# Optimization experiments

Hardware: AMD Instinct MI355X
Metric: run time of the kernel (lower is better)

## Reference

```python
import jax, jax.numpy as jnp
import numpy as np

N_NODES = 100000


def setup_inputs() -> dict:
    key = jax.random.key(0)
    k1, k2, k3, k4 = jax.random.split(key, 4)
    h = jax.random.normal(k1, (N_NODES, 128), dtype=jnp.float32)
    src = jax.random.randint(k2, (1600000,), 0, N_NODES, dtype=jnp.int32)
    dst = jax.random.randint(k3, (1600000,), 0, N_NODES, dtype=jnp.int32)
    # Linear params (PyTorch default init scale ~ 1/sqrt(in_feats))
    W = jax.random.normal(k4, (128, 128), dtype=jnp.float32) * (1.0 / np.sqrt(128.0))
    b = jnp.zeros((128,), dtype=jnp.float32)
    return {"h": h, "src": src, "dst": dst, "W": W, "b": b}


def reference(h, src, dst, W, b):
    # fn.copy_src: gather source-node features per edge  [E, F]
    msgs = h[src]
    # fn.sum: scatter-add messages into destination nodes  [N, F]
    agg = jax.ops.segment_sum(msgs, dst, num_segments=h.shape[0])
    # NodeUpdateModule: linear + relu
    out = agg @ W.T + b
    return jax.nn.relu(out)
```

## Files before the change

### kernel.cpp

```cpp
#include <hip/hip_runtime.h>

#define F      128
#define NPB    256
#define NPBS   8
#define NBMAX  512
#define ECAP   5120
#define CHMAX  4096
#define CH_PT  4
#define OVFCAP 32768
#define BR     64
#define KC     32

typedef short bf16x8 __attribute__((ext_vector_type(8)));
typedef float f32x4  __attribute__((ext_vector_type(4)));

__device__ __forceinline__ unsigned short f32_to_bf16_rne(float x) {
    unsigned u = __float_as_uint(x);
    u += 0x7fffu + ((u >> 16) & 1u);
    return (unsigned short)(u >> 16);
}
__device__ __forceinline__ float bf16_to_f32(unsigned short u) {
    return __uint_as_float((unsigned)u << 16);
}

__global__ __launch_bounds__(256) void conv_w_kernel(
        const float* __restrict__ Wf, unsigned short* __restrict__ Wb, int n4) {
    int i = blockIdx.x * blockDim.x + threadIdx.x;
    if (i < n4) {
        float4 v = *(const float4*)(Wf + 4 * (long)i);
        ushort4 o;
        o.x = f32_to_bf16_rne(v.x);
        o.y = f32_to_bf16_rne(v.y);
        o.z = f32_to_bf16_rne(v.z);
        o.w = f32_to_bf16_rne(v.w);
        *(ushort4*)(Wb + 4 * (long)i) = o;
    }
}

__global__ __launch_bounds__(256) void gemm_h_kernel(
        const float* __restrict__ h,
        const unsigned short* __restrict__ Wb,
        unsigned short* __restrict__ hp,
        int n_rows) {
    const int wave = (blockIdx.x * 256 + threadIdx.x) >> 6;
    const int lane = threadIdx.x & 63;
    const int m0 = wave * 16;
    if (m0 >= n_rows) return;
    const int mn   = lane & 15;
    const int quad = lane >> 4;

    const int rowc = min(m0 + mn, n_rows - 1);
    const float* arow = h + (long)rowc * F + quad * 8;

    bf16x8 afr[4];
    #pragma unroll
    for (int kk = 0; kk < 4; ++kk) {
        float4 p0 = *(const float4*)(arow + kk * 32);
        float4 p1 = *(const float4*)(arow + kk * 32 + 4);
        bf16x8 f;
        f[0] = (short)f32_to_bf16_rne(p0.x);
        f[1] = (short)f32_to_bf16_rne(p0.y);
        f[2] = (short)f32_to_bf16_rne(p0.z);
        f[3] = (short)f32_to_bf16_rne(p0.w);
        f[4] = (short)f32_to_bf16_rne(p1.x);
        f[5] = (short)f32_to_bf16_rne(p1.y);
        f[6] = (short)f32_to_bf16_rne(p1.z);
        f[7] = (short)f32_to_bf16_rne(p1.w);
        afr[kk] = f;
    }

    f32x4 acc[8];
    #pragma unroll
    for (int t = 0; t < 8; ++t) acc[t] = (f32x4){0.f, 0.f, 0.f, 0.f};

    #pragma unroll
    for (int kk = 0; kk < 4; ++kk) {
        #pragma unroll
        for (int t = 0; t < 8; ++t) {
            const unsigned short* wp = Wb + (long)(t * 16 + mn) * F + kk * 32 + quad * 8;
            bf16x8 bfr = *(const bf16x8*)wp;
            acc[t] = __builtin_amdgcn_mfma_f32_16x16x32_bf16(afr[kk], bfr, acc[t], 0, 0, 0);
        }
    }

    #pragma unroll
    for (int t = 0; t < 8; ++t) {
        const int col = t * 16 + mn;
        #pragma unroll
        for (int r = 0; r < 4; ++r) {
            const int orow = m0 + quad * 4 + r;
            if (orow < n_rows)
                hp[(long)orow * F + col] = f32_to_bf16_rne(acc[t][r]);
        }
    }
}

__global__ __launch_bounds__(1024) void count_kernel(
        const int* __restrict__ dst,
        int* __restrict__ cntmat,
        int n_edges, int NB) {
    __shared__ int hist[NBMAX];
    const int tid = threadIdx.x;
    const int lo = blockIdx.x * CHMAX;
    const int hi = min(n_edges, lo + CHMAX);
    for (int i = tid; i < NB; i += 1024) hist[i] = 0;
    __syncthreads();
    for (int i = lo + tid; i < hi; i += 1024)
        atomicAdd(&hist[((unsigned)dst[i]) >> NPBS], 1);
    __syncthreads();
    int* row = cntmat + (long)blockIdx.x * NB;
    for (int i = tid; i < NB; i += 1024) row[i] = hist[i];
}

__global__ __launch_bounds__(256) void scan_kernel(
        int* __restrict__ cntmat, int* __restrict__ gcnt, int NB, int NBLK) {
    __shared__ int wsum[4];
    const int b = blockIdx.x;
    const int tid = threadIdx.x;
    const int lane = tid & 63;
    const int w = tid >> 6;
    int carry = 0;
    for (int c0 = 0; c0 < NBLK; c0 += 256) {
        const int blk = c0 + tid;
        const int own = (blk < NBLK) ? cntmat[(long)blk * NB + b] : 0;
        int v = own;
        #pragma unroll
        for (int d = 1; d < 64; d <<= 1) { int u = __shfl_up(v, d); if (lane >= d) v += u; }
        if (lane == 63) wsum[w] = v;
        __syncthreads();
        if (w == 0) {
            int s = (lane < 4) ? wsum[lane] : 0;
            #pragma unroll
            for (int d = 1; d < 4; d <<= 1) { int u = __shfl_up(s, d); if (lane >= d) s += u; }
            if (lane < 4) wsum[lane] = s;
        }
        __syncthreads();
        const int excl = v - own + ((w > 0) ? wsum[w - 1] : 0) + carry;
        if (blk < NBLK) cntmat[(long)blk * NB + b] = excl;
        carry += wsum[3];
        __syncthreads();
    }
    if (tid == 0) gcnt[b] = carry;
}

__global__ __launch_bounds__(1024) void scatter_kernel(
        const int* __restrict__ src,
        const int* __restrict__ dst,
        const int* __restrict__ cntmat,
        int* __restrict__ ebuf,
        int* __restrict__ ovf,
        int n_edges, int NB) {
    __shared__ int hist[NBMAX];
    __shared__ int dlt[NBMAX];
    __shared__ int cursor[NBMAX];
    __shared__ int sval[CHMAX];
    __shared__ unsigned short sbkt[CHMAX];
    __shared__ int wsum[16];
    const int tid = threadIdx.x;
    const int lane = tid & 63;
    const int w = tid >> 6;
    const int lo = blockIdx.x * CHMAX;
    const int hi = min(n_edges, lo + CHMAX);
    const int len = hi - lo;

    int dd[CH_PT], ss[CH_PT];
    #pragma unroll
    for (int k = 0; k < CH_PT; ++k) {
        int i = lo + k * 1024 + tid;
        bool ok = i < hi;
        dd[k] = ok ? dst[i] : -1;
        ss[k] = ok ? src[i] : 0;
    }
    for (int i = tid; i < NB; i += 1024) hist[i] = 0;
    __syncthreads();

    #pragma unroll
    for (int k = 0; k < CH_PT; ++k)
        if (dd[k] >= 0) atomicAdd(&hist[((unsigned)dd[k]) >> NPBS], 1);
    __syncthreads();

    const int own = (tid < NB) ? hist[tid] : 0;
    int v = own;
    #pragma unroll
    for (int d = 1; d < 64; d <<= 1) { int u = __shfl_up(v, d); if (lane >= d) v += u; }
    if (lane == 63) wsum[w] = v;
    __syncthreads();
    if (w == 0) {
        int s = (lane < 16) ? wsum[lane] : 0;
        #pragma unroll
        for (int d = 1; d < 16; d <<= 1) { int u = __shfl_up(s, d); if (lane >= d) s += u; }
        if (lane < 16) wsum[lane] = s;
    }
    __syncthreads();
    if (tid < NB) {
        const int excl = v - own + ((w > 0) ? wsum[w - 1] : 0);
        dlt[tid] = cntmat[(long)blockIdx.x * NB + tid] - excl;
        cursor[tid] = excl;
    }
    __syncthreads();

    #pragma unroll
    for (int k = 0; k < CH_PT; ++k)
        if (dd[k] >= 0) {
            int b = ((unsigned)dd[k]) >> NPBS;
            int p = atomicAdd(&cursor[b], 1);
            sval[p] = ((dd[k] & (NPB - 1)) << 20) | ss[k];
            sbkt[p] = (unsigned short)b;
        }
    __syncthreads();

    for (int i = tid; i < len; i += 1024) {
        int vv = sval[i];
        int b = sbkt[i];
        int slot = i + dlt[b];
        if (slot < ECAP) {
            ebuf[(long)b * ECAP + slot] = vv;
        } else {
            int q = atomicAdd(&ovf[0], 1);
            if (q < OVFCAP) {
                ovf[1 + 2 * q] = (b << NPBS) | (vv >> 20);
                ovf[2 + 2 * q] = vv & 0xFFFFF;
            }
        }
    }
}

__global__ __launch_bounds__(1024) void bucket_gather_kernel(
        const unsigned short* __restrict__ hp,
        const int* __restrict__ gcnt,
        const int* __restrict__ ebuf,
        const int* __restrict__ ovf,
        const float* __restrict__ bias,
        float* __restrict__ out,
        int n_nodes) {
    __shared__ int hist[NPB];
    __shared__ int ofs[NPB];
    __shared__ int cur[NPB];
    __shared__ int srt[ECAP];
    __shared__ int wsum[16];
    const int bkt = blockIdx.x;
    const int tid = threadIdx.x;
    const int lane = tid & 63;
    const int w = tid >> 6;
    const int cnt = min(gcnt[bkt], ECAP);
    const int novf = ovf[0];
    const int* eb = ebuf + (long)bkt * ECAP;

    int ev[5];
    #pragma unroll
    for (int k = 0; k < 5; ++k) {
        int i = k * 1024 + tid;
        ev[k] = (i < cnt) ? eb[i] : -1;
    }
    if (tid < NPB) hist[tid] = 0;
    __syncthreads();

    #pragma unroll
    for (int k = 0; k < 5; ++k)
        if (ev[k] >= 0) atomicAdd(&hist[((unsigned)ev[k]) >> 20], 1);
    __syncthreads();

    const int own = (tid < NPB) ? hist[tid] : 0;
    int v = own;
    #pragma unroll
    for (int d = 1; d < 64; d <<= 1) { int u = __shfl_up(v, d); if (lane >= d) v += u; }
    if (lane == 63) wsum[w] = v;
    __syncthreads();
    if (w == 0) {
        int s = (lane < 16) ? wsum[lane] : 0;
        #pragma unroll
        for (int d = 1; d < 16; d <<= 1) { int u = __shfl_up(s, d); if (lane >= d) s += u; }
        if (lane < 16) wsum[lane] = s;
    }
    __syncthreads();
    if (tid < NPB) {
        const int e = v - own + ((w > 0) ? wsum[w - 1] : 0);
        ofs[tid] = e;
        cur[tid] = e;
    }
    __syncthreads();

    #pragma unroll
    for (int k = 0; k < 5; ++k)
        if (ev[k] >= 0) {
            int p = atomicAdd(&cur[((unsigned)ev[k]) >> 20], 1);
            srt[p] = ev[k] & 0xFFFFF;
        }
    __syncthreads();

    const unsigned lo4 = lane << 2;
    const float2 bv = *(const float2*)(bias + (lane << 1));
    for (int nl = w; nl < NPB; nl += 16) {
        const int n = (bkt << NPBS) + nl;
        if (n >= n_nodes) break;
        const int beg = ofs[nl];
        const int end = beg + hist[nl];

        float ax = 0.f, ay = 0.f;
        for (int i = beg; i < end; i += 8) {
            unsigned vv[8]; bool val[8];
            #pragma unroll
            for (int j = 0; j < 8; ++j) {
                val[j] = (i + j) < end;
                int sid = srt[val[j] ? i + j : beg];
                unsigned bo = ((unsigned)sid << 8) | lo4;
                vv[j] = *(const unsigned*)((const char*)hp + bo);
            }
            #pragma unroll
            for (int j = 0; j < 8; ++j) {
                if (val[j]) {
                    ax += __uint_as_float(vv[j] << 16);
                    ay += __uint_as_float(vv[j] & 0xffff0000u);
                }
            }
        }

        if (novf > 0) {
            int ne = min(novf, OVFCAP);
            for (int k = 0; k < ne; ++k) {
                if (ovf[1 + 2 * k] == n) {
                    int s = ovf[2 + 2 * k];
                    unsigned bo = ((unsigned)s << 8) | lo4;
                    unsigned u = *(const unsigned*)((const char*)hp + bo);
                    ax += __uint_as_float(u << 16);
                    ay += __uint_as_float(u & 0xffff0000u);
                }
            }
        }

        float rx = fmaxf(ax + bv.x, 0.f);
        float ry = fmaxf(ay + bv.y, 0.f);
        unsigned oo = ((unsigned)n << 9) | (lane << 3);
        *(float2*)((char*)out + oo) = make_float2(rx, ry);
    }
}

__global__ void scatter_add_kernel(const float* __restrict__ h,
                                   const int* __restrict__ src,
                                   const int* __restrict__ dst,
                                   float* __restrict__ agg,
                                   long total) {
    long stride = (long)gridDim.x * blockDim.x;
    for (long i = (long)blockIdx.x * blockDim.x + threadIdx.x; i < total; i += stride) {
        int e    = (int)(i >> 5);
        int lane = (int)(i & 31);
        int s = src[e];
        int d = dst[e];
        float4 v = *(const float4*)(h + (long)s * F + (lane << 2));
        float* o = agg + (long)d * F + (lane << 2);
        unsafeAtomicAdd(o + 0, v.x);
        unsafeAtomicAdd(o + 1, v.y);
        unsafeAtomicAdd(o + 2, v.z);
        unsafeAtomicAdd(o + 3, v.w);
    }
}

__global__ __launch_bounds__(256) void gemm_bias_relu_inplace(
        float* __restrict__ out,
        const float* __restrict__ W,
        const float* __restrict__ bias,
        int n_rows) {
    __shared__ __align__(16) float a_t[KC][BR + 4];
    __shared__ __align__(16) float w_t[KC][F + 4];
    const int tid = threadIdx.x;
    const int tx = tid & 15;
    const int ty = tid >> 4;
    const int row0 = blockIdx.x * BR;
    float acc[4][8];
    #pragma unroll
    for (int i = 0; i < 4; ++i)
        #pragma unroll
        for (int j = 0; j < 8; ++j) acc[i][j] = 0.f;
    for (int kc = 0; kc < F; kc += KC) {
        #pragma unroll
        for (int p = 0; p < 2; ++p) {
            int q = tid + p * 256, r = q >> 3, kq = q & 7;
            int row = row0 + r;
            float4 v = make_float4(0.f, 0.f, 0.f, 0.f);
            if (row < n_rows) v = *(const float4*)(out + (long)row * F + kc + (kq << 2));
            a_t[kq * 4 + 0][r] = v.x; a_t[kq * 4 + 1][r] = v.y;
            a_t[kq * 4 + 2][r] = v.z; a_t[kq * 4 + 3][r] = v.w;
        }
        #pragma unroll
        for (int p = 0; p < 4; ++p) {
            int q = tid + p * 256, j = q >> 3, kq = q & 7;
            float4 v = *(const float4*)(W + (long)j * F + kc + (kq << 2));
            w_t[kq * 4 + 0][j] = v.x; w_t[kq * 4 + 1][j] = v.y;
            w_t[kq * 4 + 2][j] = v.z; w_t[kq * 4 + 3][j] = v.w;
        }
        __syncthreads();
        #pragma unroll
        for (int k = 0; k < KC; ++k) {
            float4 av = *(const float4*)&a_t[k][ty << 2];
            float4 w0 = *(const float4*)&w_t[k][tx << 2];
            float4 w1 = *(const float4*)&w_t[k][64 + (tx << 2)];
            float a4[4] = {av.x, av.y, av.z, av.w};
            float wv[8] = {w0.x, w0.y, w0.z, w0.w, w1.x, w1.y, w1.z, w1.w};
            #pragma unroll
            for (int i = 0; i < 4; ++i)
                #pragma unroll
                for (int j = 0; j < 8; ++j) acc[i][j] += a4[i] * wv[j];
        }
        __syncthreads();
    }
    float4 b0 = *(const float4*)(bias + (tx << 2));
    float4 b1 = *(const float4*)(bias + 64 + (tx << 2));
    #pragma unroll
    for (int i = 0; i < 4; ++i) {
        int row = row0 + (ty << 2) + i;
        if (row < n_rows) {
            float4 r0, r1;
            r0.x = fmaxf(acc[i][0] + b0.x, 0.f); r0.y = fmaxf(acc[i][1] + b0.y, 0.f);
            r0.z = fmaxf(acc[i][2] + b0.z, 0.f); r0.w = fmaxf(acc[i][3] + b0.w, 0.f);
            r1.x = fmaxf(acc[i][4] + b1.x, 0.f); r1.y = fmaxf(acc[i][5] + b1.y, 0.f);
            r1.z = fmaxf(acc[i][6] + b1.z, 0.f); r1.w = fmaxf(acc[i][7] + b1.w, 0.f);
            *(float4*)(out + (long)row * F + (tx << 2)) = r0;
            *(float4*)(out + (long)row * F + 64 + (tx << 2)) = r1;
        }
    }
}

extern "C" void kernel_launch(void* const* d_in, const int* in_sizes, int n_in,
                              void* d_out, int out_size, void* d_ws, size_t ws_size,
                              hipStream_t stream) {
    const float* h   = (const float*)d_in[0];
    const int*   src = (const int*)d_in[1];
    const int*   dst = (const int*)d_in[2];
    const float* W   = (const float*)d_in[3];
    const float* b   = (const float*)d_in[4];
    float* out = (float*)d_out;

    const int n_nodes = in_sizes[0] / F;
    const int n_edges = in_sizes[1];
    const int NB   = (n_nodes + NPB - 1) >> NPBS;
    const int NBLK = (n_edges + CHMAX - 1) / CHMAX;

    auto al16 = [](size_t x) { return (x + 15) & ~(size_t)15; };
    const size_t off_gcnt = 0;
    const size_t off_ovf  = al16((size_t)NB * 4);
    const size_t off_cmat = al16(off_ovf + 4 + (size_t)OVFCAP * 8);
    const size_t off_ebuf = al16(off_cmat + (size_t)NBLK * NB * 4);
    const size_t off_hp   = al16(off_ebuf + (size_t)NB * ECAP * 4);
    const size_t off_wb   = al16(off_hp + (size_t)n_nodes * F * 2);
    const size_t need     = off_wb + (size_t)F * F * 2;

    if (ws_size >= need && n_nodes > 0 && NB <= NBMAX) {
        int* gcnt = (int*)((char*)d_ws + off_gcnt);
        int* ovf  = (int*)((char*)d_ws + off_ovf);
        int* cmat = (int*)((char*)d_ws + off_cmat);
        int* ebuf = (int*)((char*)d_ws + off_ebuf);
        unsigned short* hp = (unsigned short*)((char*)d_ws + off_hp);
        unsigned short* Wb = (unsigned short*)((char*)d_ws + off_wb);

        hipMemsetAsync(ovf, 0, 4, stream);

        conv_w_kernel<<<(F * F / 4 + 255) / 256, 256, 0, stream>>>(W, Wb, F * F / 4);

        gemm_h_kernel<<<(n_nodes + 63) / 64, 256, 0, stream>>>(h, Wb, hp, n_nodes);

        if (NBLK > 0)
            count_kernel<<<NBLK, 1024, 0, stream>>>(dst, cmat, n_edges, NB);

        scan_kernel<<<NB, 256, 0, stream>>>(cmat, gcnt, NB, NBLK);

        if (NBLK > 0)
            scatter_kernel<<<NBLK, 1024, 0, stream>>>(src, dst, cmat, ebuf, ovf,
                                                      n_edges, NB);

        bucket_gather_kernel<<<NB, 1024, 0, stream>>>(hp, gcnt, ebuf, ovf, b,
                                                      out, n_nodes);
    } else {
        hipMemsetAsync(out, 0, (size_t)out_size * sizeof(float), stream);
        scatter_add_kernel<<<16384, 256, 0, stream>>>(
            h, src, dst, out, (long)n_edges * 32);
        const int gblocks = (n_nodes + BR - 1) / BR;
        gemm_bias_relu_inplace<<<gblocks, 256, 0, stream>>>(out, W, b, n_nodes);
    }
}
```

Measured before the change: 220.9 us.

## Shrink buckets, precompute per-chunk scans, pad gather lists, stage GEMM tile in LDS

Halves the destination bucket size to 128 nodes and the edge chunk to 2048 edges, launching more blocks of 512 threads for the count, scatter and gather kernels. The per-chunk exclusive scan moves into the count kernel, and the global scan writes a transposed base table, so the scatter kernel no longer recomputes a histogram. Each node's edge list in the gather kernel is padded to a multiple of 8 with a sentinel pointing at a zeroed extra row of hp, which removes per-element validity checks in the inner loop. The GEMM now loads a 64-row tile of h into LDS with coalesced reads before converting it to bf16. The cost is extra workspace, more launches' worth of blocks, and some wasted gathers on padding entries.

```diff
diff --git a/kernel.cpp b/kernel.cpp
--- a/kernel.cpp
+++ b/kernel.cpp
@@ -1,15 +1,16 @@
 #include <hip/hip_runtime.h>
 
-#define F      128
-#define NPB    256
-#define NPBS   8
-#define NBMAX  512
-#define ECAP   5120
-#define CHMAX  4096
-#define CH_PT  4
-#define OVFCAP 32768
-#define BR     64
-#define KC     32
+#define F        128
+#define NPB      128
+#define NPBS     7
+#define NBMAX    1024
+#define CHMAX    2048
+#define NBLKMAX  1024
+#define ECAP     2560
+#define SRTSZ    3456
+#define OVFCAP   32768
+#define BR       64
+#define KC       32
 
 typedef short bf16x8 __attribute__((ext_vector_type(8)));
 typedef float f32x4  __attribute__((ext_vector_type(4)));
@@ -18,9 +19,6 @@
     unsigned u = __float_as_uint(x);
     u += 0x7fffu + ((u >> 16) & 1u);
     return (unsigned short)(u >> 16);
-}
-__device__ __forceinline__ float bf16_to_f32(unsigned short u) {
-    return __uint_as_float((unsigned)u << 16);
 }
 
 __global__ __launch_bounds__(256) void conv_w_kernel(
@@ -42,32 +40,38 @@
         const unsigned short* __restrict__ Wb,
         unsigned short* __restrict__ hp,
         int n_rows) {
-    const int wave = (blockIdx.x * 256 + threadIdx.x) >> 6;
-    const int lane = threadIdx.x & 63;
-    const int m0 = wave * 16;
+    __shared__ unsigned short a_lds[64][136];
+    const int tid = threadIdx.x;
+    const int r0 = blockIdx.x * 64;
+    if (r0 >= n_rows) return;
+
+    #pragma unroll 4
+    for (int k = 0; k < 32; ++k) {
+        int idx = k * 256 + tid;
+        int row = idx >> 5;
+        int c4 = idx & 31;
+        int grow = min(r0 + row, n_rows - 1);
+        float4 v = *(const float4*)(h + (long)grow * F + c4 * 4);
+        ushort4 o;
+        o.x = f32_to_bf16_rne(v.x);
+        o.y = f32_to_bf16_rne(v.y);
+        o.z = f32_to_bf16_rne(v.z);
+        o.w = f32_to_bf16_rne(v.w);
+        *(ushort4*)&a_lds[row][c4 * 4] = o;
+    }
+    __syncthreads();
+
+    const int wv = tid >> 6;
+    const int lane = tid & 63;
+    const int mn = lane & 15;
+    const int quad = lane >> 4;
+    const int m0 = r0 + wv * 16;
     if (m0 >= n_rows) return;
-    const int mn   = lane & 15;
-    const int quad = lane >> 4;
-
-    const int rowc = min(m0 + mn, n_rows - 1);
-    const float* arow = h + (long)rowc * F + quad * 8;
 
     bf16x8 afr[4];
     #pragma unroll
-    for (int kk = 0; kk < 4; ++kk) {
-        float4 p0 = *(const float4*)(arow + kk * 32);
-        float4 p1 = *(const float4*)(arow + kk * 32 + 4);
-        bf16x8 f;
-        f[0] = (short)f32_to_bf16_rne(p0.x);
-        f[1] = (short)f32_to_bf16_rne(p0.y);
-        f[2] = (short)f32_to_bf16_rne(p0.z);
-        f[3] = (short)f32_to_bf16_rne(p0.w);
-        f[4] = (short)f32_to_bf16_rne(p1.x);
-        f[5] = (short)f32_to_bf16_rne(p1.y);
-        f[6] = (short)f32_to_bf16_rne(p1.z);
-        f[7] = (short)f32_to_bf16_rne(p1.w);
-        afr[kk] = f;
-    }
+    for (int kk = 0; kk < 4; ++kk)
+        afr[kk] = *(const bf16x8*)&a_lds[wv * 16 + mn][kk * 32 + quad * 8];
 
     f32x4 acc[8];
     #pragma unroll
@@ -95,112 +99,121 @@
     }
 }
 
-__global__ __launch_bounds__(1024) void count_kernel(
+__global__ __launch_bounds__(512) void count_kernel(
         const int* __restrict__ dst,
-        int* __restrict__ cntmat,
+        int* __restrict__ cnt,
+        int* __restrict__ lexcl,
         int n_edges, int NB) {
     __shared__ int hist[NBMAX];
-    const int tid = threadIdx.x;
-    const int lo = blockIdx.x * CHMAX;
-    const int hi = min(n_edges, lo + CHMAX);
-    for (int i = tid; i < NB; i += 1024) hist[i] = 0;
-    __syncthreads();
-    for (int i = lo + tid; i < hi; i += 1024)
-        atomicAdd(&hist[((unsigned)dst[i]) >> NPBS], 1);
-    __syncthreads();
-    int* row = cntmat + (long)blockIdx.x * NB;
-    for (int i = tid; i < NB; i += 1024) row[i] = hist[i];
-}
-
-__global__ __launch_bounds__(256) void scan_kernel(
-        int* __restrict__ cntmat, int* __restrict__ gcnt, int NB, int NBLK) {
-    __shared__ int wsum[4];
-    const int b = blockIdx.x;
-    const int tid = threadIdx.x;
-    const int lane = tid & 63;
-    const int w = tid >> 6;
-    int carry = 0;
-    for (int c0 = 0; c0 < NBLK; c0 += 256) {
-        const int blk = c0 + tid;
-        const int own = (blk < NBLK) ? cntmat[(long)blk * NB + b] : 0;
-        int v = own;
-        #pragma unroll
-        for (int d = 1; d < 64; d <<= 1) { int u = __shfl_up(v, d); if (lane >= d) v += u; }
-        if (lane == 63) wsum[w] = v;
-        __syncthreads();
-        if (w == 0) {
-            int s = (lane < 4) ? wsum[lane] : 0;
-            #pragma unroll
-            for (int d = 1; d < 4; d <<= 1) { int u = __shfl_up(s, d); if (lane >= d) s += u; }
-            if (lane < 4) wsum[lane] = s;
-        }
-        __syncthreads();
-        const int excl = v - own + ((w > 0) ? wsum[w - 1] : 0) + carry;
-        if (blk < NBLK) cntmat[(long)blk * NB + b] = excl;
-        carry += wsum[3];
-        __syncthreads();
-    }
-    if (tid == 0) gcnt[b] = carry;
-}
-
-__global__ __launch_bounds__(1024) void scatter_kernel(
-        const int* __restrict__ src,
-        const int* __restrict__ dst,
-        const int* __restrict__ cntmat,
-        int* __restrict__ ebuf,
-        int* __restrict__ ovf,
-        int n_edges, int NB) {
-    __shared__ int hist[NBMAX];
-    __shared__ int dlt[NBMAX];
-    __shared__ int cursor[NBMAX];
-    __shared__ int sval[CHMAX];
-    __shared__ unsigned short sbkt[CHMAX];
-    __shared__ int wsum[16];
+    __shared__ int wsum[8];
     const int tid = threadIdx.x;
     const int lane = tid & 63;
     const int w = tid >> 6;
     const int lo = blockIdx.x * CHMAX;
     const int hi = min(n_edges, lo + CHMAX);
+
+    for (int i = tid; i < NB; i += 512) hist[i] = 0;
+    __syncthreads();
+    for (int i = lo + tid; i < hi; i += 512)
+        atomicAdd(&hist[((unsigned)dst[i]) >> NPBS], 1);
+    __syncthreads();
+
+    int* crow = cnt + (long)blockIdx.x * NB;
+    int* erow = lexcl + (long)blockIdx.x * NB;
+    int carry = 0;
+    for (int c0 = 0; c0 < NB; c0 += 512) {
+        const int idx = c0 + tid;
+        const int own = (idx < NB) ? hist[idx] : 0;
+        int v = own;
+        #pragma unroll
+        for (int d = 1; d < 64; d <<= 1) { int u = __shfl_up(v, d); if (lane >= d) v += u; }
+        if (lane == 63) wsum[w] = v;
+        __syncthreads();
+        if (w == 0) {
+            int s = (lane < 8) ? wsum[lane] : 0;
+            #pragma unroll
+            for (int d = 1; d < 8; d <<= 1) { int u = __shfl_up(s, d); if (lane >= d) s += u; }
+            if (lane < 8) wsum[lane] = s;
+        }
+        __syncthreads();
+        const int ex = v - own + ((w > 0) ? wsum[w - 1] : 0) + carry;
+        if (idx < NB) { crow[idx] = own; erow[idx] = ex; }
+        carry += wsum[7];
+        __syncthreads();
+    }
+}
+
+__global__ __launch_bounds__(256) void scan_kernel(
+        const int* __restrict__ cnt,
+        int* __restrict__ gbase,
+        int* __restrict__ gcnt,
+        int NB, int NBLK) {
+    __shared__ int wsum[4];
+    const int b = blockIdx.x;
+    const int tid = threadIdx.x;
+    const int lane = tid & 63;
+    const int w = tid >> 6;
+    int* grow = gbase + (long)b * NBLK;
+    int carry = 0;
+    for (int c0 = 0; c0 < NBLK; c0 += 256) {
+        const int c = c0 + tid;
+        const int own = (c < NBLK) ? cnt[(long)c * NB + b] : 0;
+        int v = own;
+        #pragma unroll
+        for (int d = 1; d < 64; d <<= 1) { int u = __shfl_up(v, d); if (lane >= d) v += u; }
+        if (lane == 63) wsum[w] = v;
+        __syncthreads();
+        if (w == 0) {
+            int s = (lane < 4) ? wsum[lane] : 0;
+            #pragma unroll
+            for (int d = 1; d < 4; d <<= 1) { int u = __shfl_up(s, d); if (lane >= d) s += u; }
+            if (lane < 4) wsum[lane] = s;
+        }
+        __syncthreads();
+        const int ex = v - own + ((w > 0) ? wsum[w - 1] : 0) + carry;
+        if (c < NBLK) grow[c] = ex;
+        carry += wsum[3];
+        __syncthreads();
+    }
+    if (tid == 0) gcnt[b] = carry;
+}
+
+__global__ __launch_bounds__(512) void scatter_kernel(
+        const int* __restrict__ src,
+        const int* __restrict__ dst,
+        const int* __restrict__ lexcl,
+        const int* __restrict__ gbase,
+        int* __restrict__ ebuf,
+        int* __restrict__ ovf,
+        int n_edges, int NB, int NBLK) {
+    __shared__ int cursor[NBMAX];
+    __shared__ int dlt[NBMAX];
+    __shared__ int sval[CHMAX];
+    __shared__ unsigned short sbkt[CHMAX];
+    const int tid = threadIdx.x;
+    const int ch = blockIdx.x;
+    const int lo = ch * CHMAX;
+    const int hi = min(n_edges, lo + CHMAX);
     const int len = hi - lo;
 
-    int dd[CH_PT], ss[CH_PT];
-    #pragma unroll
-    for (int k = 0; k < CH_PT; ++k) {
-        int i = lo + k * 1024 + tid;
+    int dd[4], ss[4];
+    #pragma unroll
+    for (int k = 0; k < 4; ++k) {
+        int i = lo + k * 512 + tid;
         bool ok = i < hi;
         dd[k] = ok ? dst[i] : -1;
         ss[k] = ok ? src[i] : 0;
     }
-    for (int i = tid; i < NB; i += 1024) hist[i] = 0;
-    __syncthreads();
-
-    #pragma unroll
-    for (int k = 0; k < CH_PT; ++k)
-        if (dd[k] >= 0) atomicAdd(&hist[((unsigned)dd[k]) >> NPBS], 1);
-    __syncthreads();
-
-    const int own = (tid < NB) ? hist[tid] : 0;
-    int v = own;
-    #pragma unroll
-    for (int d = 1; d < 64; d <<= 1) { int u = __shfl_up(v, d); if (lane >= d) v += u; }
-    if (lane == 63) wsum[w] = v;
-    __syncthreads();
-    if (w == 0) {
-        int s = (lane < 16) ? wsum[lane] : 0;
-        #pragma unroll
-        for (int d = 1; d < 16; d <<= 1) { int u = __shfl_up(s, d); if (lane >= d) s += u; }
-        if (lane < 16) wsum[lane] = s;
-    }
-    __syncthreads();
-    if (tid < NB) {
-        const int excl = v - own + ((w > 0) ? wsum[w - 1] : 0);
-        dlt[tid] = cntmat[(long)blockIdx.x * NB + tid] - excl;
-        cursor[tid] = excl;
-    }
-    __syncthreads();
-
-    #pragma unroll
-    for (int k = 0; k < CH_PT; ++k)
+    const int* erow = lexcl + (long)ch * NB;
+    for (int i = tid; i < NB; i += 512) {
+        int lex = erow[i];
+        cursor[i] = lex;
+        dlt[i] = gbase[(long)i * NBLK + ch] - lex;
+    }
+    __syncthreads();
+
+    #pragma unroll
+    for (int k = 0; k < 4; ++k)
         if (dd[k] >= 0) {
             int b = ((unsigned)dd[k]) >> NPBS;
             int p = atomicAdd(&cursor[b], 1);
@@ -209,7 +222,7 @@
         }
     __syncthreads();
 
-    for (int i = tid; i < len; i += 1024) {
+    for (int i = tid; i < len; i += 512) {
         int vv = sval[i];
         int b = sbkt[i];
         int slot = i + dlt[b];
@@ -225,7 +238,7 @@
     }
 }
 
-__global__ __launch_bounds__(1024) void bucket_gather_kernel(
+__global__ __launch_bounds__(512) void bucket_gather_kernel(
         const unsigned short* __restrict__ hp,
         const int* __restrict__ gcnt,
         const int* __restrict__ ebuf,
@@ -234,22 +247,22 @@
         float* __restrict__ out,
         int n_nodes) {
     __shared__ int hist[NPB];
-    __shared__ int ofs[NPB];
+    __shared__ int ofs[NPB + 1];
     __shared__ int cur[NPB];
-    __shared__ int srt[ECAP];
-    __shared__ int wsum[16];
-    const int bkt = blockIdx.x;
+    __shared__ __align__(16) int srt[SRTSZ];
+    __shared__ int wsum[8];
+    const int b = blockIdx.x;
     const int tid = threadIdx.x;
     const int lane = tid & 63;
     const int w = tid >> 6;
-    const int cnt = min(gcnt[bkt], ECAP);
+    const int cnt = min(gcnt[b], ECAP);
     const int novf = ovf[0];
-    const int* eb = ebuf + (long)bkt * ECAP;
+    const int* eb = ebuf + (long)b * ECAP;
 
     int ev[5];
     #pragma unroll
     for (int k = 0; k < 5; ++k) {
-        int i = k * 1024 + tid;
+        int i = k * 512 + tid;
         ev[k] = (i < cnt) ? eb[i] : -1;
     }
     if (tid < NPB) hist[tid] = 0;
@@ -260,23 +273,25 @@
         if (ev[k] >= 0) atomicAdd(&hist[((unsigned)ev[k]) >> 20], 1);
     __syncthreads();
 
-    const int own = (tid < NPB) ? hist[tid] : 0;
-    int v = own;
-    #pragma unroll
-    for (int d = 1; d < 64; d <<= 1) { int u = __shfl_up(v, d); if (lane >= d) v += u; }
-    if (lane == 63) wsum[w] = v;
-    __syncthreads();
-    if (w == 0) {
-        int s = (lane < 16) ? wsum[lane] : 0;
-        #pragma unroll
-        for (int d = 1; d < 16; d <<= 1) { int u = __shfl_up(s, d); if (lane >= d) s += u; }
-        if (lane < 16) wsum[lane] = s;
-    }
-    __syncthreads();
-    if (tid < NPB) {
-        const int e = v - own + ((w > 0) ? wsum[w - 1] : 0);
-        ofs[tid] = e;
-        cur[tid] = e;
+    {
+        const int own = (tid < NPB) ? hist[tid] : 0;
+        const int pd = (own + 7) & ~7;
+        int v = pd;
+        #pragma unroll
+        for (int d = 1; d < 64; d <<= 1) { int u = __shfl_up(v, d); if (lane >= d) v += u; }
+        if (lane == 63) wsum[w] = v;
+        __syncthreads();
+        if (w == 0) {
+            int s = (lane < 8) ? wsum[lane] : 0;
+            #pragma unroll
+            for (int d = 1; d < 8; d <<= 1) { int u = __shfl_up(s, d); if (lane >= d) s += u; }
+            if (lane < 8) wsum[lane] = s;
+        }
+        __syncthreads();
+        const int ex = v - pd + ((w > 0) ? wsum[w - 1] : 0);
+        if (tid < NPB) { ofs[tid] = ex; cur[tid] = ex; }
+        if (tid == NPB - 1) ofs[NPB] = ex + pd;
+        for (int i = tid; i < SRTSZ; i += 512) srt[i] = n_nodes;
     }
     __syncthreads();
 
@@ -290,28 +305,26 @@
 
     const unsigned lo4 = lane << 2;
     const float2 bv = *(const float2*)(bias + (lane << 1));
-    for (int nl = w; nl < NPB; nl += 16) {
-        const int n = (bkt << NPBS) + nl;
+    for (int nl = w; nl < NPB; nl += 8) {
+        const int n = (b << NPBS) + nl;
         if (n >= n_nodes) break;
         const int beg = ofs[nl];
-        const int end = beg + hist[nl];
+        const int pend = ofs[nl + 1];
 
         float ax = 0.f, ay = 0.f;
-        for (int i = beg; i < end; i += 8) {
-            unsigned vv[8]; bool val[8];
+        for (int i = beg; i < pend; i += 8) {
+            const int4 ia = *(const int4*)&srt[i];
+            const int4 ib = *(const int4*)&srt[i + 4];
+            int sid[8] = {ia.x, ia.y, ia.z, ia.w, ib.x, ib.y, ib.z, ib.w};
+            unsigned vv[8];
+            #pragma unroll
+            for (int j = 0; j < 8; ++j)
+                vv[j] = *(const unsigned*)((const char*)hp +
+                                           (((unsigned)sid[j] << 8) | lo4));
             #pragma unroll
             for (int j = 0; j < 8; ++j) {
-                val[j] = (i + j) < end;
-                int sid = srt[val[j] ? i + j : beg];
-                unsigned bo = ((unsigned)sid << 8) | lo4;
-                vv[j] = *(const unsigned*)((const char*)hp + bo);
-            }
-            #pragma unroll
-            for (int j = 0; j < 8; ++j) {
-                if (val[j]) {
-                    ax += __uint_as_float(vv[j] << 16);
-                    ay += __uint_as_float(vv[j] & 0xffff0000u);
-                }
+                ax += __uint_as_float(vv[j] << 16);
+                ay += __uint_as_float(vv[j] & 0xffff0000u);
             }
         }
 
@@ -319,9 +332,8 @@
             int ne = min(novf, OVFCAP);
             for (int k = 0; k < ne; ++k) {
                 if (ovf[1 + 2 * k] == n) {
-                    int s = ovf[2 + 2 * k];
-                    unsigned bo = ((unsigned)s << 8) | lo4;
-                    unsigned u = *(const unsigned*)((const char*)hp + bo);
+                    unsigned u = *(const unsigned*)((const char*)hp +
+                                   (((unsigned)ovf[2 + 2 * k] << 8) | lo4));
                     ax += __uint_as_float(u << 16);
                     ay += __uint_as_float(u & 0xffff0000u);
                 }
@@ -330,8 +342,8 @@
 
         float rx = fmaxf(ax + bv.x, 0.f);
         float ry = fmaxf(ay + bv.y, 0.f);
-        unsigned oo = ((unsigned)n << 9) | (lane << 3);
-        *(float2*)((char*)out + oo) = make_float2(rx, ry);
+        *(float2*)((char*)out + (((unsigned)n << 9) | (lane << 3))) =
+            make_float2(rx, ry);
     }
 }
 
@@ -438,37 +450,42 @@
     auto al16 = [](size_t x) { return (x + 15) & ~(size_t)15; };
     const size_t off_gcnt = 0;
     const size_t off_ovf  = al16((size_t)NB * 4);
-    const size_t off_cmat = al16(off_ovf + 4 + (size_t)OVFCAP * 8);
-    const size_t off_ebuf = al16(off_cmat + (size_t)NBLK * NB * 4);
+    const size_t off_cnt  = al16(off_ovf + 4 + (size_t)OVFCAP * 8);
+    const size_t off_lex  = al16(off_cnt + (size_t)NBLK * NB * 4);
+    const size_t off_gb   = al16(off_lex + (size_t)NBLK * NB * 4);
+    const size_t off_ebuf = al16(off_gb + (size_t)NB * NBLK * 4);
     const size_t off_hp   = al16(off_ebuf + (size_t)NB * ECAP * 4);
-    const size_t off_wb   = al16(off_hp + (size_t)n_nodes * F * 2);
+    const size_t off_wb   = al16(off_hp + (size_t)(n_nodes + 1) * F * 2);
     const size_t need     = off_wb + (size_t)F * F * 2;
 
-    if (ws_size >= need && n_nodes > 0 && NB <= NBMAX) {
-        int* gcnt = (int*)((char*)d_ws + off_gcnt);
-        int* ovf  = (int*)((char*)d_ws + off_ovf);
-        int* cmat = (int*)((char*)d_ws + off_cmat);
-        int* ebuf = (int*)((char*)d_ws + off_ebuf);
+    if (ws_size >= need && n_nodes > 0 && NB <= NBMAX && NBLK <= NBLKMAX) {
+        int* gcnt  = (int*)((char*)d_ws + off_gcnt);
+        int* ovf   = (int*)((char*)d_ws + off_ovf);
+        int* cnt   = (int*)((char*)d_ws + off_cnt);
+        int* lexcl = (int*)((char*)d_ws + off_lex);
+        int* gbase = (int*)((char*)d_ws + off_gb);
+        int* ebuf  = (int*)((char*)d_ws + off_ebuf);
         unsigned short* hp = (unsigned short*)((char*)d_ws + off_hp);
         unsigned short* Wb = (unsigned short*)((char*)d_ws + off_wb);
 
         hipMemsetAsync(ovf, 0, 4, stream);
+        hipMemsetAsync(hp + (size_t)n_nodes * F, 0, (size_t)F * 2, stream);
 
         conv_w_kernel<<<(F * F / 4 + 255) / 256, 256, 0, stream>>>(W, Wb, F * F / 4);
 
         gemm_h_kernel<<<(n_nodes + 63) / 64, 256, 0, stream>>>(h, Wb, hp, n_nodes);
 
         if (NBLK > 0)
-            count_kernel<<<NBLK, 1024, 0, stream>>>(dst, cmat, n_edges, NB);
-
-        scan_kernel<<<NB, 256, 0, stream>>>(cmat, gcnt, NB, NBLK);
+            count_kernel<<<NBLK, 512, 0, stream>>>(dst, cnt, lexcl, n_edges, NB);
+
+        scan_kernel<<<NB, 256, 0, stream>>>(cnt, gbase, gcnt, NB, NBLK);
 
         if (NBLK > 0)
-            scatter_kernel<<<NBLK, 1024, 0, stream>>>(src, dst, cmat, ebuf, ovf,
-                                                      n_edges, NB);
-
-        bucket_gather_kernel<<<NB, 1024, 0, stream>>>(hp, gcnt, ebuf, ovf, b,
-                                                      out, n_nodes);
+            scatter_kernel<<<NBLK, 512, 0, stream>>>(src, dst, lexcl, gbase,
+                                                     ebuf, ovf, n_edges, NB, NBLK);
+
+        bucket_gather_kernel<<<NB, 512, 0, stream>>>(hp, gcnt, ebuf, ovf, b,
+                                                     out, n_nodes);
     } else {
         hipMemsetAsync(out, 0, (size_t)out_size * sizeof(float), stream);
         scatter_add_kernel<<<16384, 256, 0, stream>>>(
```

Result: slower. 255.0 us (+15.4%).
